# Performance work log

Measured on AMD Instinct MI355X. Metric: run time of the kernel, lower is better.

The kernel has to match this reference:

```python
import jax, jax.numpy as jnp
import numpy as np

B, C, H, W = 16, 256, 64, 64   # img feature map -> S = H*W = 4096 query tokens
L, TXT = 256, 256              # text tokens / text_dim
NH, HD = 4, 64                 # fusion_num_heads, fusion_head_dim -> embed_dim 256
E = NH * HD


def layernorm(x, w, b, eps=1e-5):
    mu = x.mean(-1, keepdims=True)
    var = ((x - mu) ** 2).mean(-1, keepdims=True)
    return (x - mu) * jax.lax.rsqrt(var + eps) * w + b


def setup_inputs() -> dict:
    key = jax.random.key(0)
    ks = jax.random.split(key, 10)
    s = 0.02  # xavier-ish init scale
    return {
        "img_x": jax.random.normal(ks[0], (B, C, H, W), jnp.float32),
        "refs": jax.random.normal(ks[1], (B, L, TXT), jnp.float32),
        "masks": jax.random.bernoulli(ks[2], 0.2, (B, L)),  # True = padded token
        "ref_embeds": jax.random.normal(ks[3], (B, C), jnp.float32),
        "ln_img_w": jnp.ones((C,), jnp.float32),
        "ln_img_b": jnp.zeros((C,), jnp.float32),
        "ln_txt_w": jnp.ones((TXT,), jnp.float32),
        "ln_txt_b": jnp.zeros((TXT,), jnp.float32),
        "Wq": jax.random.normal(ks[4], (C, E), jnp.float32) * s,
        "bq": jnp.zeros((E,), jnp.float32),
        "Wk": jax.random.normal(ks[5], (TXT, E), jnp.float32) * s,
        "bk": jnp.zeros((E,), jnp.float32),
        "Wv": jax.random.normal(ks[6], (TXT, E), jnp.float32) * s,
        "bv": jnp.zeros((E,), jnp.float32),
        "Wo": jax.random.normal(ks[7], (E, C), jnp.float32) * s,
        "bo": jnp.zeros((C,), jnp.float32),
        "W_ada": jax.random.normal(ks[8], (C, 3 * C), jnp.float32) * s,
        "b_ada": jnp.zeros((3 * C,), jnp.float32),
    }


def reference(img_x, refs, masks, ref_embeds,
              ln_img_w, ln_img_b, ln_txt_w, ln_txt_b,
              Wq, bq, Wk, bk, Wv, bv, Wo, bo, W_ada, b_ada):
    B_, C_, H_, W_ = img_x.shape
    x = img_x.reshape(B_, C_, H_ * W_).transpose(0, 2, 1)  # [B, S, C]

    qn = layernorm(x, ln_img_w, ln_img_b)
    kn = layernorm(refs, ln_txt_w, ln_txt_b)

    q = (qn @ Wq + bq).reshape(B_, -1, NH, HD).astype(jnp.bfloat16)
    k = (kn @ Wk + bk).reshape(B_, -1, NH, HD).astype(jnp.bfloat16)
    v = (kn @ Wv + bv).reshape(B_, -1, NH, HD).astype(jnp.bfloat16)

    scale = 1.0 / np.sqrt(HD).astype(np.float32)
    scores = jnp.einsum('bqhd,bkhd->bhqk', q, k).astype(jnp.float32) * scale
    valid = ~masks  # unpad_input keeps keys where (~masks)==1
    scores = jnp.where(valid[:, None, None, :], scores, -jnp.inf)
    p = jax.nn.softmax(scores, axis=-1).astype(jnp.bfloat16)
    o = jnp.einsum('bhqk,bkhd->bqhd', p, v).reshape(B_, -1, E).astype(jnp.float32)
    attn = o @ Wo + bo  # [B, S, C]

    # AdaLN shift/scale/gate modulation from ref_embeds
    mod = jax.nn.silu(ref_embeds) @ W_ada + b_ada  # [B, 3C]
    shift, sc, gate = jnp.split(mod, 3, axis=1)
    attn = gate[:, None, :] * (attn * (1.0 + sc[:, None, :]) + shift[:, None, :])

    out = (attn + x).transpose(0, 2, 1).reshape(B_, C_, H_, W_)
    return out
```

## Files before the change

### kernel.cpp

```cpp
#include <hip/hip_runtime.h>
#include <hip/hip_bf16.h>

#define NB 16
#define NC 256
#define NS 4096
#define NL 256
#define NE 256
#define NHH 4
#define HDD 64

using bf16 = __hip_bfloat16;
typedef short bf16x8 __attribute__((ext_vector_type(8)));
typedef float f32x4 __attribute__((ext_vector_type(4)));

__device__ __forceinline__ float bf16r(float x) {
    return __bfloat162float(__float2bfloat16(x));
}
__device__ __forceinline__ float rsqrt_nr(float x) {
    float r = rsqrtf(x);
    r = r * (1.5f - 0.5f * x * r * r);
    return r;
}
__device__ __forceinline__ ushort us(float x) {
    bf16 h = __float2bfloat16(x);
    return *(ushort*)&h;
}

__global__ void __launch_bounds__(256) wt_kernel(const float* __restrict__ Wq,
                                                 const float* __restrict__ Wk,
                                                 const float* __restrict__ Wv,
                                                 const float* __restrict__ Wo,
                                                 ushort* __restrict__ wqt,
                                                 ushort* __restrict__ wkt,
                                                 ushort* __restrict__ wvt,
                                                 ushort* __restrict__ wot) {
    int m = blockIdx.x >> 3, strip = blockIdx.x & 7;
    const float* W = (m == 0) ? Wq : (m == 1) ? Wk : (m == 2) ? Wv : Wo;
    ushort* Wt = (m == 0) ? wqt : (m == 1) ? wkt : (m == 2) ? wvt : wot;
    int t = threadIdx.x;
    __shared__ float tile[32 * 257];
    int in0 = strip * 32;
    for (int i = 0; i < 32; i++) tile[i * 257 + t] = W[(size_t)(in0 + i) * 256 + t];
    __syncthreads();
    ushort vals[32];
#pragma unroll
    for (int i = 0; i < 32; i++) vals[i] = us(tile[i * 257 + t]);
#pragma unroll
    for (int i = 0; i < 32; i += 8)
        *(uint4*)(Wt + (size_t)t * 256 + in0 + i) = *(const uint4*)(vals + i);
}

__global__ void __launch_bounds__(256) mod_kernel(const float* __restrict__ ref_embeds,
                                                  const float* __restrict__ W_ada,
                                                  const float* __restrict__ b_ada,
                                                  float* __restrict__ mod) {
    int b = blockIdx.x / 12, jc = blockIdx.x % 12;
    int t = threadIdx.x;
    __shared__ float silu[NC];
    __shared__ float part[256];
    float x = ref_embeds[b * NC + t];
    silu[t] = x / (1.f + expf(-x));
    __syncthreads();
    int j = jc * 64 + (t & 63);
    int cq = t >> 6;
    float acc = 0.f;
#pragma unroll 8
    for (int c = cq * 64; c < cq * 64 + 64; c++) acc += silu[c] * W_ada[c * 3 * NC + j];
    part[t] = acc;
    __syncthreads();
    if (t < 64) {
        mod[b * 3 * NC + j] = part[t] + part[t + 64] + part[t + 128] + part[t + 192] + b_ada[j];
    }
}

__global__ void __launch_bounds__(256) kv_kernel(const float* __restrict__ refs,
                                                 const float* __restrict__ lw,
                                                 const float* __restrict__ lb,
                                                 const ushort* __restrict__ Wkt,
                                                 const float* __restrict__ bk,
                                                 const ushort* __restrict__ Wvt,
                                                 const float* __restrict__ bv,
                                                 bf16* __restrict__ kbuf,
                                                 bf16* __restrict__ vbuf) {
    int blk = blockIdx.x;
    int b = blk >> 2;
    int l0 = (blk & 3) << 6;
    int t = threadIdx.x;
    __shared__ ushort At[64 * 264];
    __shared__ float lws[NC], lbs[NC];
    lws[t] = lw[t];
    lbs[t] = lb[t];
    int r = t >> 2, j = t & 3;
    const float* rp = refs + ((size_t)(b * NL + l0 + r)) * NC + j * 64;
    float v[64];
#pragma unroll
    for (int i = 0; i < 16; i++) {
        float4 f = *(const float4*)(rp + i * 4);
        v[i * 4 + 0] = f.x; v[i * 4 + 1] = f.y; v[i * 4 + 2] = f.z; v[i * 4 + 3] = f.w;
    }
    float s = 0;
#pragma unroll
    for (int i = 0; i < 64; i++) s += v[i];
    s += __shfl_xor(s, 1, 64);
    s += __shfl_xor(s, 2, 64);
    float mu = s * (1.f / NC);
    float vr = 0;
#pragma unroll
    for (int i = 0; i < 64; i++) {
        float d = v[i] - mu;
        vr += d * d;
    }
    vr += __shfl_xor(vr, 1, 64);
    vr += __shfl_xor(vr, 2, 64);
    float rs = rsqrt_nr(vr * (1.f / NC) + 1e-5f);
    __syncthreads();
    ushort nv[64];
#pragma unroll
    for (int i = 0; i < 64; i++) {
        int c = j * 64 + i;
        nv[i] = us((v[i] - mu) * rs * lws[c] + lbs[c]);
    }
#pragma unroll
    for (int i = 0; i < 64; i += 4)
        *(uint2*)(At + r * 264 + j * 64 + i) = *(const uint2*)(nv + i);
    __syncthreads();

    int w = t >> 6, lane = t & 63, l16 = lane & 15, quad = lane >> 4;
    int r0 = w * 16;
    f32x4 zero = {0.f, 0.f, 0.f, 0.f};
    f32x4 ak[16], av[16];
#pragma unroll
    for (int et = 0; et < 16; et++) { ak[et] = zero; av[et] = zero; }
    const ushort* ap = At + (r0 + l16) * 264 + quad * 8;
    const ushort* kp = Wkt + (size_t)l16 * NC + quad * 8;
    const ushort* vp = Wvt + (size_t)l16 * NC + quad * 8;
#pragma unroll
    for (int kc = 0; kc < 8; kc++) {
        bf16x8 a = *(const bf16x8*)(ap + kc * 32);
#pragma unroll
        for (int et = 0; et < 16; et++) {
            bf16x8 bbk = *(const bf16x8*)(kp + (size_t)et * 16 * NC + kc * 32);
            ak[et] = __builtin_amdgcn_mfma_f32_16x16x32_bf16(a, bbk, ak[et], 0, 0, 0);
        }
#pragma unroll
        for (int et = 0; et < 16; et++) {
            bf16x8 bbv = *(const bf16x8*)(vp + (size_t)et * 16 * NC + kc * 32);
            av[et] = __builtin_amdgcn_mfma_f32_16x16x32_bf16(a, bbv, av[et], 0, 0, 0);
        }
    }
#pragma unroll
    for (int et = 0; et < 16; et++) {
        int e = et * 16 + l16;
        float bkv = bk[e], bvv = bv[e];
#pragma unroll
        for (int rr = 0; rr < 4; rr++) {
            size_t row = (size_t)(b * NL + l0 + r0 + quad * 4 + rr);
            kbuf[row * NE + e] = __float2bfloat16(ak[et][rr] + bkv);
            vbuf[row * NE + e] = __float2bfloat16(av[et][rr] + bvv);
        }
    }
}

__global__ void __launch_bounds__(256) vt_kernel(const bf16* __restrict__ vbuf,
                                                 ushort* __restrict__ vtbuf) {
    int bh = blockIdx.x;
    int b = bh >> 2, h = bh & 3;
    int t = threadIdx.x;
    __shared__ ushort tile[64 * 264];
    const ushort* vp = (const ushort*)vbuf + ((size_t)b * NL) * NE + h * HDD;
#pragma unroll
    for (int i = 0; i < 8; i++) {
        int l = i * 32 + (t >> 3);
        uint4 v = *(const uint4*)(vp + (size_t)l * NE + (t & 7) * 8);
        const ushort* v8 = (const ushort*)&v;
#pragma unroll
        for (int j = 0; j < 8; j++) tile[((t & 7) * 8 + j) * 264 + l] = v8[j];
    }
    __syncthreads();
    ushort* op = vtbuf + (size_t)bh * HDD * NL;
#pragma unroll
    for (int i = 0; i < 8; i++) {
        int d = i * 8 + (t >> 5);
        int l = (t & 31) * 8;
        *(uint4*)(op + (size_t)d * NL + l) = *(const uint4*)(tile + d * 264 + l);
    }
}

__global__ void __launch_bounds__(256, 2) q_kernel(const float* __restrict__ img_x,
                                                   const float* __restrict__ lw,
                                                   const float* __restrict__ lb,
                                                   const ushort* __restrict__ Wqt,
                                                   const float* __restrict__ bq,
                                                   bf16* __restrict__ qbuf) {
    int blk = blockIdx.x;
    int b = blk >> 6;
    int s0 = (blk & 63) << 6;
    int t = threadIdx.x;
    int cg = t >> 4, s4 = t & 15;

    __shared__ __attribute__((aligned(16))) char At[64 * 512];
    __shared__ float part_s[16 * 64], part_q[16 * 64];
    __shared__ float mu_s[64], rs_s[64];
    __shared__ float lws[NC], lbs[NC];
    lws[t] = lw[t];
    lbs[t] = lb[t];

    const float* xp = img_x + ((size_t)b * NC) * NS + s0 + s4 * 4;
    float4 v4[16];
#pragma unroll
    for (int i = 0; i < 16; i++) v4[i] = *(const float4*)(xp + (size_t)(i * 16 + cg) * NS);
    float ss0 = 0.f, ss1 = 0.f, ss2 = 0.f, ss3 = 0.f;
    float qq0 = 0.f, qq1 = 0.f, qq2 = 0.f, qq3 = 0.f;
#pragma unroll
    for (int i = 0; i < 16; i++) {
        ss0 += v4[i].x; qq0 += v4[i].x * v4[i].x;
        ss1 += v4[i].y; qq1 += v4[i].y * v4[i].y;
        ss2 += v4[i].z; qq2 += v4[i].z * v4[i].z;
        ss3 += v4[i].w; qq3 += v4[i].w * v4[i].w;
    }
    float4 ssv = {ss0, ss1, ss2, ss3};
    float4 qqv = {qq0, qq1, qq2, qq3};
    *(float4*)&part_s[cg * 64 + s4 * 4] = ssv;
    *(float4*)&part_q[cg * 64 + s4 * 4] = qqv;
    __syncthreads();

    if (t < 64) {
        float sm = 0.f, sq = 0.f;
#pragma unroll
        for (int g = 0; g < 16; g++) {
            sm += part_s[g * 64 + t];
            sq += part_q[g * 64 + t];
        }
        float mu = sm * (1.f / NC);
        mu_s[t] = mu;
        rs_s[t] = rsqrt_nr(sq * (1.f / NC) - mu * mu + 1e-5f);
    }
    __syncthreads();

    float mus[4], rss[4];
#pragma unroll
    for (int r = 0; r < 4; r++) {
        mus[r] = mu_s[s4 * 4 + r];
        rss[r] = rs_s[s4 * 4 + r];
    }
#pragma unroll
    for (int i = 0; i < 16; i++) {
        int c = i * 16 + cg;
        float wv = lws[c], bv_ = lbs[c];
        float xs[4] = {v4[i].x, v4[i].y, v4[i].z, v4[i].w};
#pragma unroll
        for (int r = 0; r < 4; r++) {
            int s = s4 * 4 + r;
            int sw = (((s ^ (s >> 3)) & 7) << 4);
            *(ushort*)(At + ((s * 512 + c * 2) ^ sw)) = us((xs[r] - mus[r]) * rss[r] * wv + bv_);
        }
    }
    __syncthreads();

    int w = t >> 6, lane = t & 63, l16 = lane & 15, quad = lane >> 4;
    int r0 = w * 16;
    int arow = r0 + l16;
    int asw = (((arow ^ (arow >> 3)) & 7) << 4);
    f32x4 zero = {0.f, 0.f, 0.f, 0.f};
    f32x4 acc[16];
#pragma unroll
    for (int et = 0; et < 16; et++) acc[et] = zero;
    const ushort* bp = Wqt + (size_t)l16 * NC + quad * 8;
#pragma unroll
    for (int kc = 0; kc < 8; kc++) {
        bf16x8 a = *(const bf16x8*)(At + ((arow * 512 + kc * 64 + quad * 16) ^ asw));
#pragma unroll
        for (int et = 0; et < 16; et++) {
            bf16x8 bb = *(const bf16x8*)(bp + (size_t)et * 16 * NC + kc * 32);
            acc[et] = __builtin_amdgcn_mfma_f32_16x16x32_bf16(a, bb, acc[et], 0, 0, 0);
        }
    }
#pragma unroll
    for (int et = 0; et < 16; et++) {
        int e = et * 16 + l16;
        float bqv = bq[e];
#pragma unroll
        for (int rr = 0; rr < 4; rr++) {
            int s = s0 + r0 + quad * 4 + rr;
            qbuf[((size_t)b * NS + s) * NE + e] = __float2bfloat16(acc[et][rr] + bqv);
        }
    }
}

__global__ void __launch_bounds__(256) attn_kernel(const bf16* __restrict__ qbuf,
                                                   const bf16* __restrict__ kbuf,
                                                   const ushort* __restrict__ vtbuf,
                                                   const int* __restrict__ masks,
                                                   bf16* __restrict__ obuf) {
    int blk = blockIdx.x;
    int chunk = blk & 7;
    int bh = blk >> 3;
    int h = bh & 3;
    int b = bh >> 2;
    int t = threadIdx.x;
    int w = t >> 6, lane = t & 63;
    int l16 = lane & 15, quad = lane >> 4;

    __shared__ __attribute__((aligned(16))) char sK[32768];
    __shared__ __attribute__((aligned(16))) char sV[32768];

    const char* kgb = (const char*)kbuf + ((size_t)(b * NL) * NE + h * HDD) * 2;
    const char* vgb = (const char*)vtbuf + (size_t)bh * HDD * NL * 2;
#pragma unroll
    for (int i = 0; i < 8; i++) {
        int g = t * 16 + i * 4096;
        uint4 kv = *(const uint4*)(kgb + (size_t)(g >> 7) * 512 + (g & 127));
        *(uint4*)(sK + (g ^ (((g >> 7) & 7) << 4))) = kv;
        uint4 vv = *(const uint4*)(vgb + g);
        *(uint4*)(sV + (g ^ (((g >> 9) & 7) << 4))) = vv;
    }

    const int* mp = masks + b * NL;
    unsigned long long bal0 = __ballot(mp[lane] != 0);
    unsigned long long bal1 = __ballot(mp[64 + lane] != 0);
    unsigned long long bal2 = __ballot(mp[128 + lane] != 0);
    unsigned long long bal3 = __ballot(mp[192 + lane] != 0);
    uint mw0 = 0, mw1 = 0;
#pragma unroll
    for (int kk = 0; kk < 4; kk++) {
        mw0 |= (uint)((bal0 >> (16 * kk + 4 * quad)) & 15ULL) << (4 * kk);
        mw0 |= (uint)((bal1 >> (16 * kk + 4 * quad)) & 15ULL) << (4 * kk + 16);
        mw1 |= (uint)((bal2 >> (16 * kk + 4 * quad)) & 15ULL) << (4 * kk);
        mw1 |= (uint)((bal3 >> (16 * kk + 4 * quad)) & 15ULL) << (4 * kk + 16);
    }

    int sbase = chunk * 512;
    const ushort* qp0 = (const ushort*)qbuf +
                        ((size_t)(b * NS + sbase + w * 16 + l16)) * NE + h * HDD + quad * 8;
    bf16x8 af0 = *(const bf16x8*)qp0;
    bf16x8 af1 = *(const bf16x8*)(qp0 + 32);

    __syncthreads();

    int kswz = (l16 & 7) << 4;
    int src0 = l16 + 32 * (quad & 1);
    int src1 = src0 + 16;
    bool ahi = quad >= 2;

    for (int it = 0; it < 8; it++) {
        int s0 = sbase + it * 64;
        bf16x8 nf0, nf1;
        if (it < 7) {
            const ushort* qn = qp0 + (size_t)(it + 1) * 64 * NE;
            nf0 = *(const bf16x8*)qn;
            nf1 = *(const bf16x8*)(qn + 32);
        }

        f32x4 acc[16];
#pragma unroll
        for (int kt = 0; kt < 16; kt++) {
            int row = kt * 16 + l16;
            bf16x8 kf0 = *(const bf16x8*)(sK + ((row * 128 + quad * 16) ^ kswz));
            bf16x8 kf1 = *(const bf16x8*)(sK + ((row * 128 + quad * 16 + 64) ^ kswz));
            f32x4 z = {0.f, 0.f, 0.f, 0.f};
            z = __builtin_amdgcn_mfma_f32_16x16x32_bf16(kf0, af0, z, 0, 0, 0);
            acc[kt] = __builtin_amdgcn_mfma_f32_16x16x32_bf16(kf1, af1, z, 0, 0, 0);
        }

        float srow = 0.f;
#pragma unroll
        for (int kt = 0; kt < 16; kt++) {
            uint nib = ((kt < 8) ? mw0 : mw1) >> (4 * (kt & 7));
#pragma unroll
            for (int r = 0; r < 4; r++) {
                float p = exp2f(bf16r(acc[kt][r]) * 0.18033688f);
                p = ((nib >> r) & 1) ? 0.f : p;
                acc[kt][r] = p;
                srow += p;
            }
        }
        srow += __shfl_xor(srow, 16, 64);
        srow += __shfl_xor(srow, 32, 64);
        float inv = 1.f / srow;

        uint Wloc[32];
#pragma unroll
        for (int kt = 0; kt < 16; kt++) {
            Wloc[2 * kt] = (uint)us(acc[kt][0] * inv) | ((uint)us(acc[kt][1] * inv) << 16);
            Wloc[2 * kt + 1] = (uint)us(acc[kt][2] * inv) | ((uint)us(acc[kt][3] * inv) << 16);
        }

        f32x4 oacc[4];
#pragma unroll
        for (int dt = 0; dt < 4; dt++) oacc[dt] = f32x4{0.f, 0.f, 0.f, 0.f};
#pragma unroll
        for (int kc = 0; kc < 8; kc++) {
            uint a0 = (uint)__shfl((int)Wloc[4 * kc + 0], src0, 64);
            uint b0 = (uint)__shfl((int)Wloc[4 * kc + 2], src0, 64);
            uint a1 = (uint)__shfl((int)Wloc[4 * kc + 1], src0, 64);
            uint b1 = (uint)__shfl((int)Wloc[4 * kc + 3], src0, 64);
            uint a2 = (uint)__shfl((int)Wloc[4 * kc + 0], src1, 64);
            uint b2 = (uint)__shfl((int)Wloc[4 * kc + 2], src1, 64);
            uint a3 = (uint)__shfl((int)Wloc[4 * kc + 1], src1, 64);
            uint b3 = (uint)__shfl((int)Wloc[4 * kc + 3], src1, 64);
            union { uint u[4]; bf16x8 v; } pu;
            pu.u[0] = ahi ? b0 : a0;
            pu.u[1] = ahi ? b1 : a1;
            pu.u[2] = ahi ? b2 : a2;
            pu.u[3] = ahi ? b3 : a3;
#pragma unroll
            for (int dt = 0; dt < 4; dt++) {
                int row = dt * 16 + l16;
                bf16x8 vb = *(const bf16x8*)(sV + ((row * 512 + kc * 64 + quad * 16) ^ kswz));
                oacc[dt] = __builtin_amdgcn_mfma_f32_16x16x32_bf16(pu.v, vb, oacc[dt], 0, 0, 0);
            }
        }

        bf16* op = obuf + ((size_t)(b * NS + s0 + w * 16 + quad * 4)) * NE + h * HDD + l16;
#pragma unroll
        for (int dt = 0; dt < 4; dt++) {
#pragma unroll
            for (int r = 0; r < 4; r++)
                op[(size_t)r * NE + dt * 16] = __float2bfloat16(oacc[dt][r]);
        }
        if (it < 7) { af0 = nf0; af1 = nf1; }
    }
}

__global__ void __launch_bounds__(256) out_kernel(const bf16* __restrict__ obuf,
                                                  const ushort* __restrict__ Wot,
                                                  const float* __restrict__ bo,
                                                  const float* __restrict__ mod,
                                                  const float* __restrict__ img_x,
                                                  float* __restrict__ out) {
    int blk = blockIdx.x;
    int b = blk >> 6;
    int s0 = (blk & 63) << 6;
    int t = threadIdx.x;
    int w = t >> 6, lane = t & 63, l16 = lane & 15, quad = lane >> 4;
    int c0 = w * 64;

    f32x4 zero = {0.f, 0.f, 0.f, 0.f};
    f32x4 acc[4][4];
#pragma unroll
    for (int ct = 0; ct < 4; ct++)
#pragma unroll
        for (int st = 0; st < 4; st++) acc[ct][st] = zero;

    const ushort* ap0 = Wot + (size_t)(c0 + l16) * NE + quad * 8;
    const ushort* bp0 = (const ushort*)obuf + ((size_t)(b * NS + s0 + l16)) * NE + quad * 8;
#pragma unroll
    for (int kc = 0; kc < 8; kc++) {
        bf16x8 a[4], bb[4];
#pragma unroll
        for (int ct = 0; ct < 4; ct++)
            a[ct] = *(const bf16x8*)(ap0 + (size_t)ct * 16 * NE + kc * 32);
#pragma unroll
        for (int st = 0; st < 4; st++)
            bb[st] = *(const bf16x8*)(bp0 + (size_t)st * 16 * NE + kc * 32);
#pragma unroll
        for (int ct = 0; ct < 4; ct++)
#pragma unroll
            for (int st = 0; st < 4; st++)
                acc[ct][st] = __builtin_amdgcn_mfma_f32_16x16x32_bf16(a[ct], bb[st], acc[ct][st], 0, 0, 0);
    }

#pragma unroll
    for (int ct = 0; ct < 4; ct++) {
#pragma unroll
        for (int r = 0; r < 4; r++) {
            int c = c0 + ct * 16 + quad * 4 + r;
            float sh = mod[b * 768 + c];
            float scv = mod[b * 768 + 256 + c];
            float ga = mod[b * 768 + 512 + c];
            float bov = bo[c];
            const float* xr = img_x + ((size_t)(b * NC + c)) * NS + s0;
            float* orow = out + ((size_t)(b * NC + c)) * NS + s0;
#pragma unroll
            for (int st = 0; st < 4; st++) {
                float y = ga * ((acc[ct][st][r] + bov) * (1.f + scv) + sh) + xr[st * 16 + l16];
                orow[st * 16 + l16] = y;
            }
        }
    }
}

extern "C" void kernel_launch(void* const* d_in, const int* in_sizes, int n_in,
                              void* d_out, int out_size, void* d_ws, size_t ws_size,
                              hipStream_t stream) {
    const float* img_x = (const float*)d_in[0];
    const float* refs = (const float*)d_in[1];
    const int* masks = (const int*)d_in[2];
    const float* ref_embeds = (const float*)d_in[3];
    const float* ln_img_w = (const float*)d_in[4];
    const float* ln_img_b = (const float*)d_in[5];
    const float* ln_txt_w = (const float*)d_in[6];
    const float* ln_txt_b = (const float*)d_in[7];
    const float* Wq = (const float*)d_in[8];
    const float* bq = (const float*)d_in[9];
    const float* Wk = (const float*)d_in[10];
    const float* bk = (const float*)d_in[11];
    const float* Wv = (const float*)d_in[12];
    const float* bv = (const float*)d_in[13];
    const float* Wo = (const float*)d_in[14];
    const float* bo = (const float*)d_in[15];
    const float* W_ada = (const float*)d_in[16];
    const float* b_ada = (const float*)d_in[17];
    float* out = (float*)d_out;

    char* ws = (char*)d_ws;
    float* mod = (float*)ws;
    ushort* wqt = (ushort*)(ws + 49152);
    ushort* wkt = (ushort*)(ws + 180224);
    ushort* wvt = (ushort*)(ws + 311296);
    ushort* wot = (ushort*)(ws + 442368);
    bf16* kbuf = (bf16*)(ws + 573440);
    ushort* vtbuf = (ushort*)(ws + 2670592);
    bf16* qbuf = (bf16*)(ws + 4767744);
    bf16* obuf = (bf16*)(ws + 38322176);
    bf16* vbuf = obuf;

    hipLaunchKernelGGL(wt_kernel, dim3(32), dim3(256), 0, stream,
                       Wq, Wk, Wv, Wo, wqt, wkt, wvt, wot);
    hipLaunchKernelGGL(mod_kernel, dim3(NB * 12), dim3(256), 0, stream,
                       ref_embeds, W_ada, b_ada, mod);
    hipLaunchKernelGGL(kv_kernel, dim3(NB * 4), dim3(256), 0, stream,
                       refs, ln_txt_w, ln_txt_b, wkt, bk, wvt, bv, kbuf, vbuf);
    hipLaunchKernelGGL(vt_kernel, dim3(NB * NHH), dim3(256), 0, stream,
                       vbuf, vtbuf);
    hipLaunchKernelGGL(q_kernel, dim3(NB * 64), dim3(256), 0, stream,
                       img_x, ln_img_w, ln_img_b, wqt, bq, qbuf);
    hipLaunchKernelGGL(attn_kernel, dim3(NB * NHH * 8), dim3(256), 0, stream,
                       qbuf, kbuf, vtbuf, masks, obuf);
    hipLaunchKernelGGL(out_kernel, dim3(NB * (NS / 64)), dim3(256), 0, stream,
                       obuf, wot, bo, mod, img_x, out);
}
```

Before: 401.7 us.

## Split Q projection into LayerNorm-transpose kernel and LDS-staged MFMA GEMM

Replaces the fused LayerNorm+Q-projection kernel with two kernels. The first normalizes img_x and writes a transposed bf16 [B,S,C] buffer, reusing the obuf workspace. The second runs a GEMM that stages half of the transposed Wq in swizzled LDS and computes a 128x128 output tile per block, with each wave handling 32 rows. The aim is to stop every MFMA re-reading Wq from global memory and to raise B-operand reuse. The cost is an extra read and write of the normalized activations and img_x being read twice inside the LN kernel.

```diff
diff --git a/kernel.cpp b/kernel.cpp
--- a/kernel.cpp
+++ b/kernel.cpp
@@ -186,103 +186,150 @@
     }
 }
 
-__global__ void __launch_bounds__(256, 2) q_kernel(const float* __restrict__ img_x,
-                                                   const float* __restrict__ lw,
-                                                   const float* __restrict__ lb,
-                                                   const ushort* __restrict__ Wqt,
-                                                   const float* __restrict__ bq,
-                                                   bf16* __restrict__ qbuf) {
+__global__ void __launch_bounds__(256) xln_kernel(const float* __restrict__ img_x,
+                                                  const float* __restrict__ lw,
+                                                  const float* __restrict__ lb,
+                                                  ushort* __restrict__ xq) {
     int blk = blockIdx.x;
-    int b = blk >> 6;
-    int s0 = (blk & 63) << 6;
-    int t = threadIdx.x;
-    int cg = t >> 4, s4 = t & 15;
-
-    __shared__ __attribute__((aligned(16))) char At[64 * 512];
-    __shared__ float part_s[16 * 64], part_q[16 * 64];
-    __shared__ float mu_s[64], rs_s[64];
+    int b = blk >> 4;
+    int sb = (blk & 15) << 8;
+    int t = threadIdx.x;
+    int l63 = t & 63, wq = t >> 6;
+    __shared__ float part_s[4][256], part_q[4][256];
+    __shared__ float mu_s[256], rs_s[256];
+    __shared__ ushort tile[256 * 66];
     __shared__ float lws[NC], lbs[NC];
     lws[t] = lw[t];
     lbs[t] = lb[t];
 
-    const float* xp = img_x + ((size_t)b * NC) * NS + s0 + s4 * 4;
-    float4 v4[16];
-#pragma unroll
-    for (int i = 0; i < 16; i++) v4[i] = *(const float4*)(xp + (size_t)(i * 16 + cg) * NS);
-    float ss0 = 0.f, ss1 = 0.f, ss2 = 0.f, ss3 = 0.f;
-    float qq0 = 0.f, qq1 = 0.f, qq2 = 0.f, qq3 = 0.f;
-#pragma unroll
-    for (int i = 0; i < 16; i++) {
-        ss0 += v4[i].x; qq0 += v4[i].x * v4[i].x;
-        ss1 += v4[i].y; qq1 += v4[i].y * v4[i].y;
-        ss2 += v4[i].z; qq2 += v4[i].z * v4[i].z;
-        ss3 += v4[i].w; qq3 += v4[i].w * v4[i].w;
-    }
-    float4 ssv = {ss0, ss1, ss2, ss3};
-    float4 qqv = {qq0, qq1, qq2, qq3};
-    *(float4*)&part_s[cg * 64 + s4 * 4] = ssv;
-    *(float4*)&part_q[cg * 64 + s4 * 4] = qqv;
-    __syncthreads();
-
-    if (t < 64) {
-        float sm = 0.f, sq = 0.f;
-#pragma unroll
-        for (int g = 0; g < 16; g++) {
-            sm += part_s[g * 64 + t];
-            sq += part_q[g * 64 + t];
-        }
+    const float* xb = img_x + (size_t)b * NC * NS + sb;
+    float s0 = 0.f, s1 = 0.f, s2 = 0.f, s3 = 0.f;
+    float q0 = 0.f, q1 = 0.f, q2 = 0.f, q3 = 0.f;
+    for (int it = 0; it < 64; it++) {
+        int c = it * 4 + wq;
+        float4 v = *(const float4*)(xb + (size_t)c * NS + l63 * 4);
+        s0 += v.x; q0 += v.x * v.x;
+        s1 += v.y; q1 += v.y * v.y;
+        s2 += v.z; q2 += v.z * v.z;
+        s3 += v.w; q3 += v.w * v.w;
+    }
+    part_s[wq][l63 * 4 + 0] = s0; part_q[wq][l63 * 4 + 0] = q0;
+    part_s[wq][l63 * 4 + 1] = s1; part_q[wq][l63 * 4 + 1] = q1;
+    part_s[wq][l63 * 4 + 2] = s2; part_q[wq][l63 * 4 + 2] = q2;
+    part_s[wq][l63 * 4 + 3] = s3; part_q[wq][l63 * 4 + 3] = q3;
+    __syncthreads();
+    {
+        float sm = part_s[0][t] + part_s[1][t] + part_s[2][t] + part_s[3][t];
+        float sq = part_q[0][t] + part_q[1][t] + part_q[2][t] + part_q[3][t];
         float mu = sm * (1.f / NC);
         mu_s[t] = mu;
         rs_s[t] = rsqrt_nr(sq * (1.f / NC) - mu * mu + 1e-5f);
     }
     __syncthreads();
-
-    float mus[4], rss[4];
-#pragma unroll
-    for (int r = 0; r < 4; r++) {
-        mus[r] = mu_s[s4 * 4 + r];
-        rss[r] = rs_s[s4 * 4 + r];
-    }
-#pragma unroll
-    for (int i = 0; i < 16; i++) {
-        int c = i * 16 + cg;
-        float wv = lws[c], bv_ = lbs[c];
-        float xs[4] = {v4[i].x, v4[i].y, v4[i].z, v4[i].w};
-#pragma unroll
-        for (int r = 0; r < 4; r++) {
-            int s = s4 * 4 + r;
-            int sw = (((s ^ (s >> 3)) & 7) << 4);
-            *(ushort*)(At + ((s * 512 + c * 2) ^ sw)) = us((xs[r] - mus[r]) * rss[r] * wv + bv_);
-        }
-    }
-    __syncthreads();
-
+    float4 mu4 = *(const float4*)&mu_s[l63 * 4];
+    float4 rs4 = *(const float4*)&rs_s[l63 * 4];
+    for (int ch = 0; ch < 4; ch++) {
+#pragma unroll
+        for (int it2 = 0; it2 < 16; it2++) {
+            int cl = it2 * 4 + wq;
+            int c = ch * 64 + cl;
+            float4 v = *(const float4*)(xb + (size_t)c * NS + l63 * 4);
+            float wv = lws[c], bb = lbs[c];
+            tile[(l63 * 4 + 0) * 66 + cl] = us((v.x - mu4.x) * rs4.x * wv + bb);
+            tile[(l63 * 4 + 1) * 66 + cl] = us((v.y - mu4.y) * rs4.y * wv + bb);
+            tile[(l63 * 4 + 2) * 66 + cl] = us((v.z - mu4.z) * rs4.z * wv + bb);
+            tile[(l63 * 4 + 3) * 66 + cl] = us((v.w - mu4.w) * rs4.w * wv + bb);
+        }
+        __syncthreads();
+        ushort* xrow = xq + ((size_t)(b * NS + sb)) * NC + ch * 64 + (t & 7) * 8;
+#pragma unroll
+        for (int i = 0; i < 8; i++) {
+            int s = i * 32 + (t >> 3);
+            const ushort* tp = tile + s * 66 + (t & 7) * 8;
+            uint u0 = *(const uint*)(tp);
+            uint u1 = *(const uint*)(tp + 2);
+            uint u2 = *(const uint*)(tp + 4);
+            uint u3 = *(const uint*)(tp + 6);
+            uint4 uu = {u0, u1, u2, u3};
+            *(uint4*)(xrow + (size_t)s * NC) = uu;
+        }
+        __syncthreads();
+    }
+}
+
+__global__ void __launch_bounds__(256, 2) qmm_kernel(const ushort* __restrict__ xq,
+                                                     const ushort* __restrict__ Wqt,
+                                                     const float* __restrict__ bq,
+                                                     bf16* __restrict__ qbuf) {
+    int blk = blockIdx.x;
+    int b = blk >> 6;
+    int rc = (blk >> 1) & 31;
+    int eh = blk & 1;
+    int t = threadIdx.x;
     int w = t >> 6, lane = t & 63, l16 = lane & 15, quad = lane >> 4;
-    int r0 = w * 16;
-    int arow = r0 + l16;
-    int asw = (((arow ^ (arow >> 3)) & 7) << 4);
+    int r0 = rc * 128 + w * 32;
+    int e0 = eh * 128;
+
+    __shared__ __attribute__((aligned(16))) char sB[65536];
+
+    const char* ab = (const char*)xq + ((size_t)(b * NS + r0 + l16)) * 512 + quad * 16;
+    bf16x8 a[2][8];
+#pragma unroll
+    for (int rt = 0; rt < 2; rt++)
+#pragma unroll
+        for (int kc = 0; kc < 8; kc++)
+            a[rt][kc] = *(const bf16x8*)(ab + (size_t)rt * 16 * 512 + kc * 64);
+
+    const char* wsrc = (const char*)(Wqt + (size_t)e0 * NC);
+#pragma unroll
+    for (int ii = 0; ii < 2; ii++) {
+        uint4 tmp[8];
+#pragma unroll
+        for (int j = 0; j < 8; j++) {
+            int g = ((ii * 8 + j) * 256 + t) * 16;
+            tmp[j] = *(const uint4*)(wsrc + g);
+        }
+#pragma unroll
+        for (int j = 0; j < 8; j++) {
+            int g = ((ii * 8 + j) * 256 + t) * 16;
+            *(uint4*)(sB + (g ^ (((g >> 9) & 7) << 4))) = tmp[j];
+        }
+    }
+    __syncthreads();
+
     f32x4 zero = {0.f, 0.f, 0.f, 0.f};
-    f32x4 acc[16];
-#pragma unroll
-    for (int et = 0; et < 16; et++) acc[et] = zero;
-    const ushort* bp = Wqt + (size_t)l16 * NC + quad * 8;
+    f32x4 acc[2][8];
+#pragma unroll
+    for (int rt = 0; rt < 2; rt++)
+#pragma unroll
+        for (int et = 0; et < 8; et++) acc[rt][et] = zero;
+    int swz = (l16 & 7) << 4;
 #pragma unroll
     for (int kc = 0; kc < 8; kc++) {
-        bf16x8 a = *(const bf16x8*)(At + ((arow * 512 + kc * 64 + quad * 16) ^ asw));
-#pragma unroll
-        for (int et = 0; et < 16; et++) {
-            bf16x8 bb = *(const bf16x8*)(bp + (size_t)et * 16 * NC + kc * 32);
-            acc[et] = __builtin_amdgcn_mfma_f32_16x16x32_bf16(a, bb, acc[et], 0, 0, 0);
-        }
-    }
-#pragma unroll
-    for (int et = 0; et < 16; et++) {
-        int e = et * 16 + l16;
+        bf16x8 bB[8];
+#pragma unroll
+        for (int et = 0; et < 8; et++) {
+            int e = et * 16 + l16;
+            bB[et] = *(const bf16x8*)(sB + e * 512 + ((quad * 16 + kc * 64) ^ swz));
+        }
+#pragma unroll
+        for (int et = 0; et < 8; et++) {
+#pragma unroll
+            for (int rt = 0; rt < 2; rt++)
+                acc[rt][et] = __builtin_amdgcn_mfma_f32_16x16x32_bf16(a[rt][kc], bB[et], acc[rt][et], 0, 0, 0);
+        }
+    }
+#pragma unroll
+    for (int et = 0; et < 8; et++) {
+        int e = e0 + et * 16 + l16;
         float bqv = bq[e];
 #pragma unroll
-        for (int rr = 0; rr < 4; rr++) {
-            int s = s0 + r0 + quad * 4 + rr;
-            qbuf[((size_t)b * NS + s) * NE + e] = __float2bfloat16(acc[et][rr] + bqv);
+        for (int rt = 0; rt < 2; rt++) {
+#pragma unroll
+            for (int rr = 0; rr < 4; rr++) {
+                int s = r0 + rt * 16 + quad * 4 + rr;
+                qbuf[((size_t)(b * NS + s)) * NE + e] = __float2bfloat16(acc[rt][et][rr] + bqv);
+            }
         }
     }
 }
@@ -514,6 +561,7 @@
     bf16* qbuf = (bf16*)(ws + 4767744);
     bf16* obuf = (bf16*)(ws + 38322176);
     bf16* vbuf = obuf;
+    ushort* xq = (ushort*)obuf;
 
     hipLaunchKernelGGL(wt_kernel, dim3(32), dim3(256), 0, stream,
                        Wq, Wk, Wv, Wo, wqt, wkt, wvt, wot);
@@ -523,8 +571,10 @@
                        refs, ln_txt_w, ln_txt_b, wkt, bk, wvt, bv, kbuf, vbuf);
     hipLaunchKernelGGL(vt_kernel, dim3(NB * NHH), dim3(256), 0, stream,
                        vbuf, vtbuf);
-    hipLaunchKernelGGL(q_kernel, dim3(NB * 64), dim3(256), 0, stream,
-                       img_x, ln_img_w, ln_img_b, wqt, bq, qbuf);
+    hipLaunchKernelGGL(xln_kernel, dim3(NB * 16), dim3(256), 0, stream,
+                       img_x, ln_img_w, ln_img_b, xq);
+    hipLaunchKernelGGL(qmm_kernel, dim3(NB * 64), dim3(256), 0, stream,
+                       xq, wqt, bq, qbuf);
     hipLaunchKernelGGL(attn_kernel, dim3(NB * NHH * 8), dim3(256), 0, stream,
                        qbuf, kbuf, vtbuf, masks, obuf);
     hipLaunchKernelGGL(out_kernel, dim3(NB * (NS / 64)), dim3(256), 0, stream,
```

After: 370.8 us. 1.08x faster.
